# Optimization experiments

Hardware: AMD Instinct MI355X
Metric: run time of the kernel (lower is better)

The kernel has to match this reference:

```python
import jax, jax.numpy as jnp
import numpy as np

N, C, H = 256, 128, 4
D = C // H


def setup_inputs() -> dict:
    key = jax.random.key(0)
    ks = jax.random.split(key, 7)
    pair_rep = jax.random.normal(ks[0], (N, N, C), dtype=jnp.float32)
    distance_matrix = jax.random.normal(ks[1], (N, N), dtype=jnp.float32)
    Wqkv = jax.random.normal(ks[2], (C, 3 * C), dtype=jnp.float32) * (1.0 / np.sqrt(C))
    bqkv = jax.random.normal(ks[3], (3 * C,), dtype=jnp.float32) * 0.02
    Wout = jax.random.normal(ks[4], (C, C), dtype=jnp.float32) * (1.0 / np.sqrt(C))
    bout = jax.random.normal(ks[5], (C,), dtype=jnp.float32) * 0.02
    dscale = jnp.ones((1,), dtype=jnp.float32)
    mask = jax.random.randint(ks[6], (N, N), 0, 2).astype(jnp.bool_)
    return {"pair_rep": pair_rep, "distance_matrix": distance_matrix, "Wqkv": Wqkv,
            "bqkv": bqkv, "Wout": Wout, "bout": bout, "dscale": dscale, "mask": mask}


def reference(pair_rep, distance_matrix, Wqkv, bqkv, Wout, bout, dscale, mask):
    n = pair_rep.shape[0]
    qkv = pair_rep @ Wqkv + bqkv                      # [n,n,3c]
    q, k, v = jnp.split(qkv, 3, axis=-1)
    q = q.reshape(n, n, H, D)
    k = k.reshape(n, n, H, D)
    v = v.reshape(n, n, H, D)
    # scores[h,i,j,k] = q[i,j,h,:] . k[i,k,h,:] / sqrt(D)
    scores = jnp.einsum('ijhd,ikhd->hijk', q, k) / np.sqrt(D)
    bias = (dscale[0] * distance_matrix)[None, None, :, :]   # [1,1,n,n]
    scores = scores + bias
    scores = jnp.where(mask[None, None, :, :], -jnp.inf, scores)
    attn = jax.nn.softmax(scores, axis=-1)            # [H,n,n,n]
    out = jnp.einsum('hijk,ikhd->ijhd', attn, v).reshape(n, n, C)
    return out @ Wout + bout
```

## Files before the change

kernel.cpp:

```cpp
#include <hip/hip_runtime.h>
#include <hip/hip_bf16.h>
#include <math.h>

#define NN 256
#define CC 128
#define HH 4
#define DD 32

typedef uint4 u128;
typedef __bf16 bf16x8 __attribute__((ext_vector_type(8)));
typedef float f32x4 __attribute__((ext_vector_type(4)));

#define LOG2E 1.4426950408889634f
#define QSC (0.17677669529663687f * LOG2E)

__global__ __launch_bounds__(256) void prep_kernel(
    const float* __restrict__ dm, const int* __restrict__ mask,
    const float* __restrict__ dscale,
    const float* __restrict__ Wqkv, const float* __restrict__ Wout,
    float* __restrict__ bias2,
    __hip_bfloat16* __restrict__ Wt_qkv, __hip_bfloat16* __restrict__ Wt_out)
{
    const int b = blockIdx.x, t = threadIdx.x;
    if (b < 256) {
        const int j = b, k = t;
        int idx = j * 256 + k;
        float v = mask[idx] ? -INFINITY : dscale[0] * dm[idx] * LOG2E;
        int c = k >> 5, bb = (k >> 4) & 1, quad = (k >> 2) & 3, r = k & 3;
        int dst = ((((c * 2 + bb) * 16 + (j >> 4)) * 64) + quad * 16 + (j & 15)) * 4 + r;
        bias2[dst] = v;
    } else if (b < 448) {
        int idx = (b - 256) * 256 + t;
        int n = idx >> 7, k = idx & 127;
        Wt_qkv[idx] = __float2bfloat16(Wqkv[(size_t)k * 384 + n]);
    } else {
        int idx = (b - 448) * 256 + t;
        int n = idx >> 7, k = idx & 127;
        Wt_out[idx] = __float2bfloat16(Wout[(size_t)k * CC + n]);
    }
}

__global__ __launch_bounds__(512, 4) void qkv_mfma_kernel(
    const float* __restrict__ A,
    const __hip_bfloat16* __restrict__ Bt,
    const float* __restrict__ bias,
    __hip_bfloat16* __restrict__ out)
{
    __shared__ __align__(16) __hip_bfloat16 As[128][136];
    __shared__ __align__(16) __hip_bfloat16 Bs[96][136];
    const int t = threadIdx.x;
    const int m0 = blockIdx.x * 128;
    const int n0 = blockIdx.y * 96;

    #pragma unroll
    for (int it = 0; it < 8; ++it) {
        int idx = it * 512 + t;
        int r = idx >> 5, c4 = (idx & 31) * 4;
        float4 v = *(const float4*)(A + (size_t)(m0 + r) * CC + c4);
        __hip_bfloat162 a01 = __float22bfloat162_rn(float2{v.x, v.y});
        __hip_bfloat162 a23 = __float22bfloat162_rn(float2{v.z, v.w});
        uint2 pk;
        pk.x = *(unsigned int*)&a01;
        pk.y = *(unsigned int*)&a23;
        *(uint2*)&As[r][c4] = pk;
    }
    #pragma unroll
    for (int it = 0; it < 3; ++it) {
        int idx = it * 512 + t;
        int n = idx >> 4, c8 = (idx & 15) * 8;
        *(u128*)&Bs[n][c8] = *(const u128*)(Bt + (size_t)(n0 + n) * CC + c8);
    }
    __syncthreads();

    const int w = t >> 6, lane = t & 63;
    const int n16 = lane & 15, quad = lane >> 4;
    const int mw = (w & 3) * 32, nw = (w >> 2) * 48;

    bf16x8 pf[2][4];
    #pragma unroll
    for (int mt = 0; mt < 2; ++mt)
        #pragma unroll
        for (int ks = 0; ks < 4; ++ks)
            pf[mt][ks] = *(const bf16x8*)&As[mw + mt * 16 + n16][ks * 32 + quad * 8];

    f32x4 acc[2][3];
    #pragma unroll
    for (int mt = 0; mt < 2; ++mt)
        #pragma unroll
        for (int nt = 0; nt < 3; ++nt) acc[mt][nt] = (f32x4){0.f, 0.f, 0.f, 0.f};

    #pragma unroll
    for (int nt = 0; nt < 3; ++nt) {
        bf16x8 wf[4];
        #pragma unroll
        for (int ks = 0; ks < 4; ++ks)
            wf[ks] = *(const bf16x8*)&Bs[nw + nt * 16 + n16][ks * 32 + quad * 8];
        #pragma unroll
        for (int ks = 0; ks < 4; ++ks)
            #pragma unroll
            for (int mt = 0; mt < 2; ++mt)
                acc[mt][nt] = __builtin_amdgcn_mfma_f32_16x16x32_bf16(wf[ks], pf[mt][ks], acc[mt][nt], 0, 0, 0);
    }

    #pragma unroll
    for (int nt = 0; nt < 3; ++nt) {
        int nbase = n0 + nw + nt * 16 + quad * 4;
        float4 b4 = *(const float4*)(bias + nbase);
        float sc = (nbase < CC) ? QSC : 1.0f;
        #pragma unroll
        for (int mt = 0; mt < 2; ++mt) {
            int m = m0 + mw + mt * 16 + n16;
            __hip_bfloat162 h01 = __float22bfloat162_rn(float2{(acc[mt][nt][0] + b4.x) * sc, (acc[mt][nt][1] + b4.y) * sc});
            __hip_bfloat162 h23 = __float22bfloat162_rn(float2{(acc[mt][nt][2] + b4.z) * sc, (acc[mt][nt][3] + b4.w) * sc});
            uint2 pk;
            pk.x = *(unsigned int*)&h01;
            pk.y = *(unsigned int*)&h23;
            *(uint2*)&out[(size_t)m * 384 + nbase] = pk;
        }
    }
}

__global__ __launch_bounds__(512, 8) void attn_mfma_kernel(
    const __hip_bfloat16* __restrict__ qkv,
    const float* __restrict__ bias2,
    __hip_bfloat16* __restrict__ attn_out)
{
    __shared__ __align__(16) __hip_bfloat16 Ks[NN][40];
    __shared__ __align__(16) __hip_bfloat16 VTs[DD][264];

    const int bi = blockIdx.x;
    const int i = bi >> 2, h = bi & 3;
    const int t = threadIdx.x;

    {
        const int r = t >> 1, half = t & 1;
        const __hip_bfloat16* base = qkv + (size_t)(i * NN + r) * 384 + h * DD;
        const u128* ksrc = (const u128*)(base + CC) + half * 2;
        u128* kdst = (u128*)&Ks[r][0] + half * 2;
        kdst[0] = ksrc[0];
        kdst[1] = ksrc[1];
        const u128* vsrc = (const u128*)(base + 2 * CC) + half * 2;
        u128 vr[2];
        vr[0] = vsrc[0];
        vr[1] = vsrc[1];
        const __hip_bfloat16* vh = (const __hip_bfloat16*)vr;
        const int pr = (r & ~0x1F) | ((r & 0xC) << 1) | ((r & 0x10) >> 2) | (r & 0x3);
        #pragma unroll
        for (int dd = 0; dd < 16; ++dd) VTs[half * 16 + dd][pr] = vh[dd];
    }
    __syncthreads();

    const int w = t >> 6, lane = t & 63;
    const int n16 = lane & 15, quad = lane >> 4;

    #pragma unroll
    for (int jt = 0; jt < 2; ++jt) {
        const int j0 = w * 32 + jt * 16;
        const int j = j0 + n16;
        const int jblk = w * 2 + jt;

        bf16x8 qa = *(const bf16x8*)(qkv + (size_t)(i * NN + j) * 384 + h * DD + quad * 8);
        const float4* bb = (const float4*)bias2;

        f32x4 sm = {0.f, 0.f, 0.f, 0.f};
        f32x4 o0 = {0.f, 0.f, 0.f, 0.f}, o1 = {0.f, 0.f, 0.f, 0.f};

        #pragma unroll 2
        for (int c = 0; c < 8; ++c) {
            float4 b0 = bb[((c * 2 + 0) * 16 + jblk) * 64 + lane];
            float4 b1 = bb[((c * 2 + 1) * 16 + jblk) * 64 + lane];
            bf16x8 kb0 = *(const bf16x8*)&Ks[c * 32 + n16][quad * 8];
            bf16x8 kb1 = *(const bf16x8*)&Ks[c * 32 + 16 + n16][quad * 8];
            f32x4 s0 = __builtin_amdgcn_mfma_f32_16x16x32_bf16(
                kb0, qa, (f32x4){b0.x, b0.y, b0.z, b0.w}, 0, 0, 0);
            f32x4 s1 = __builtin_amdgcn_mfma_f32_16x16x32_bf16(
                kb1, qa, (f32x4){b1.x, b1.y, b1.z, b1.w}, 0, 0, 0);

            float p0 = __builtin_amdgcn_exp2f(s0[0]);
            float p1 = __builtin_amdgcn_exp2f(s0[1]);
            float p2 = __builtin_amdgcn_exp2f(s0[2]);
            float p3 = __builtin_amdgcn_exp2f(s0[3]);
            float p4 = __builtin_amdgcn_exp2f(s1[0]);
            float p5 = __builtin_amdgcn_exp2f(s1[1]);
            float p6 = __builtin_amdgcn_exp2f(s1[2]);
            float p7 = __builtin_amdgcn_exp2f(s1[3]);
            sm[0] += p0 + p4;
            sm[1] += p1 + p5;
            sm[2] += p2 + p6;
            sm[3] += p3 + p7;

            __hip_bfloat162 q01 = __float22bfloat162_rn(float2{p0, p1});
            __hip_bfloat162 q23 = __float22bfloat162_rn(float2{p2, p3});
            __hip_bfloat162 q45 = __float22bfloat162_rn(float2{p4, p5});
            __hip_bfloat162 q67 = __float22bfloat162_rn(float2{p6, p7});
            u128 pk;
            pk.x = *(unsigned int*)&q01;
            pk.y = *(unsigned int*)&q23;
            pk.z = *(unsigned int*)&q45;
            pk.w = *(unsigned int*)&q67;
            bf16x8 pa = *(bf16x8*)&pk;

            bf16x8 vb0 = *(const bf16x8*)&VTs[n16][c * 32 + quad * 8];
            bf16x8 vb1 = *(const bf16x8*)&VTs[16 + n16][c * 32 + quad * 8];
            o0 = __builtin_amdgcn_mfma_f32_16x16x32_bf16(vb0, pa, o0, 0, 0, 0);
            o1 = __builtin_amdgcn_mfma_f32_16x16x32_bf16(vb1, pa, o1, 0, 0, 0);
        }

        float sum = (sm[0] + sm[1]) + (sm[2] + sm[3]);
        sum += __shfl_xor(sum, 16);
        sum += __shfl_xor(sum, 32);
        float inv = 1.0f / sum;

        __hip_bfloat16* obase = attn_out + (size_t)(i * NN + j) * CC + h * DD + quad * 4;
        {
            __hip_bfloat162 h01 = __float22bfloat162_rn(float2{o0[0] * inv, o0[1] * inv});
            __hip_bfloat162 h23 = __float22bfloat162_rn(float2{o0[2] * inv, o0[3] * inv});
            uint2 pk;
            pk.x = *(unsigned int*)&h01;
            pk.y = *(unsigned int*)&h23;
            *(uint2*)(obase) = pk;
        }
        {
            __hip_bfloat162 h01 = __float22bfloat162_rn(float2{o1[0] * inv, o1[1] * inv});
            __hip_bfloat162 h23 = __float22bfloat162_rn(float2{o1[2] * inv, o1[3] * inv});
            uint2 pk;
            pk.x = *(unsigned int*)&h01;
            pk.y = *(unsigned int*)&h23;
            *(uint2*)(obase + 16) = pk;
        }
    }
}

__global__ __launch_bounds__(512, 4) void out_mfma_kernel(
    const __hip_bfloat16* __restrict__ A,
    const __hip_bfloat16* __restrict__ Bt,
    const float* __restrict__ bias,
    float* __restrict__ out)
{
    __shared__ __align__(16) __hip_bfloat16 As[128][136];
    __shared__ __align__(16) __hip_bfloat16 Bs[128][136];
    const int t = threadIdx.x;
    const int m0 = blockIdx.x * 128;

    #pragma unroll
    for (int it = 0; it < 4; ++it) {
        int idx = it * 512 + t;
        int r = idx >> 4, c8 = (idx & 15) * 8;
        *(u128*)&As[r][c8] = *(const u128*)(A + (size_t)(m0 + r) * CC + c8);
    }
    #pragma unroll
    for (int it = 0; it < 4; ++it) {
        int idx = it * 512 + t;
        int n = idx >> 4, c8 = (idx & 15) * 8;
        *(u128*)&Bs[n][c8] = *(const u128*)(Bt + (size_t)n * CC + c8);
    }
    __syncthreads();

    const int w = t >> 6, lane = t & 63;
    const int n16 = lane & 15, quad = lane >> 4;
    const int mw = (w & 3) * 32, nw = (w >> 2) * 64;

    bf16x8 pf[2][4];
    #pragma unroll
    for (int mt = 0; mt < 2; ++mt)
        #pragma unroll
        for (int ks = 0; ks < 4; ++ks)
            pf[mt][ks] = *(const bf16x8*)&As[mw + mt * 16 + n16][ks * 32 + quad * 8];

    f32x4 acc[2][4];
    #pragma unroll
    for (int mt = 0; mt < 2; ++mt)
        #pragma unroll
        for (int nt = 0; nt < 4; ++nt) acc[mt][nt] = (f32x4){0.f, 0.f, 0.f, 0.f};

    #pragma unroll
    for (int nt = 0; nt < 4; ++nt) {
        bf16x8 wf[4];
        #pragma unroll
        for (int ks = 0; ks < 4; ++ks)
            wf[ks] = *(const bf16x8*)&Bs[nw + nt * 16 + n16][ks * 32 + quad * 8];
        #pragma unroll
        for (int ks = 0; ks < 4; ++ks)
            #pragma unroll
            for (int mt = 0; mt < 2; ++mt)
                acc[mt][nt] = __builtin_amdgcn_mfma_f32_16x16x32_bf16(wf[ks], pf[mt][ks], acc[mt][nt], 0, 0, 0);
    }

    #pragma unroll
    for (int nt = 0; nt < 4; ++nt) {
        int nbase = nw + nt * 16 + quad * 4;
        float4 b4 = *(const float4*)(bias + nbase);
        #pragma unroll
        for (int mt = 0; mt < 2; ++mt) {
            int m = m0 + mw + mt * 16 + n16;
            float4 ov;
            ov.x = acc[mt][nt][0] + b4.x;
            ov.y = acc[mt][nt][1] + b4.y;
            ov.z = acc[mt][nt][2] + b4.z;
            ov.w = acc[mt][nt][3] + b4.w;
            *(float4*)&out[(size_t)m * CC + nbase] = ov;
        }
    }
}

extern "C" void kernel_launch(void* const* d_in, const int* in_sizes, int n_in,
                              void* d_out, int out_size, void* d_ws, size_t ws_size,
                              hipStream_t stream) {
    const float* pair_rep = (const float*)d_in[0];
    const float* dm       = (const float*)d_in[1];
    const float* Wqkv     = (const float*)d_in[2];
    const float* bqkv     = (const float*)d_in[3];
    const float* Wout     = (const float*)d_in[4];
    const float* bout     = (const float*)d_in[5];
    const float* dscale   = (const float*)d_in[6];
    const int*   mask     = (const int*)d_in[7];
    float* out = (float*)d_out;

    char* p = (char*)d_ws;
    float* bias2 = (float*)p;                 p += (size_t)NN * NN * 4;
    __hip_bfloat16* Wt_qkv = (__hip_bfloat16*)p;  p += (size_t)384 * CC * 2;
    __hip_bfloat16* Wt_out = (__hip_bfloat16*)p;  p += (size_t)CC * CC * 2;
    __hip_bfloat16* qkv  = (__hip_bfloat16*)p;    p += (size_t)65536 * 384 * 2;
    __hip_bfloat16* attn = (__hip_bfloat16*)p;

    prep_kernel<<<dim3(512), dim3(256), 0, stream>>>(dm, mask, dscale, Wqkv, Wout, bias2, Wt_qkv, Wt_out);
    qkv_mfma_kernel<<<dim3(512, 4), dim3(512), 0, stream>>>(pair_rep, Wt_qkv, bqkv, qkv);
    attn_mfma_kernel<<<dim3(1024), dim3(512), 0, stream>>>(qkv, bias2, attn);
    out_mfma_kernel<<<dim3(512), dim3(512), 0, stream>>>(attn, Wt_out, bout, out);
}
```

Baseline: 160.8 us.

## Load A tile once per QKV block and loop over output column chunks

The QKV projection grid drops from 512x4 to 512 blocks. Each block converts its fp32 input rows to bf16 in shared memory once, then loops over the four 96-column weight chunks, prefetching the next chunk into registers while writing the current outputs. This removes the fourfold re-read of the fp32 pair representation. Global loads in the QKV and output GEMMs are also batched into registers before the shared-memory stores to increase memory-level parallelism. The cost is fewer blocks, more serial work per block, and a lower occupancy hint.

```diff
diff --git a/kernel.cpp b/kernel.cpp
--- a/kernel.cpp
+++ b/kernel.cpp
@@ -40,7 +40,7 @@
     }
 }
 
-__global__ __launch_bounds__(512, 4) void qkv_mfma_kernel(
+__global__ __launch_bounds__(512, 2) void qkv_mfma_kernel(
     const float* __restrict__ A,
     const __hip_bfloat16* __restrict__ Bt,
     const float* __restrict__ bias,
@@ -50,15 +50,20 @@
     __shared__ __align__(16) __hip_bfloat16 Bs[96][136];
     const int t = threadIdx.x;
     const int m0 = blockIdx.x * 128;
-    const int n0 = blockIdx.y * 96;
-
+
+    float4 va[8];
     #pragma unroll
     for (int it = 0; it < 8; ++it) {
         int idx = it * 512 + t;
         int r = idx >> 5, c4 = (idx & 31) * 4;
-        float4 v = *(const float4*)(A + (size_t)(m0 + r) * CC + c4);
-        __hip_bfloat162 a01 = __float22bfloat162_rn(float2{v.x, v.y});
-        __hip_bfloat162 a23 = __float22bfloat162_rn(float2{v.z, v.w});
+        va[it] = *(const float4*)(A + (size_t)(m0 + r) * CC + c4);
+    }
+    #pragma unroll
+    for (int it = 0; it < 8; ++it) {
+        int idx = it * 512 + t;
+        int r = idx >> 5, c4 = (idx & 31) * 4;
+        __hip_bfloat162 a01 = __float22bfloat162_rn(float2{va[it].x, va[it].y});
+        __hip_bfloat162 a23 = __float22bfloat162_rn(float2{va[it].z, va[it].w});
         uint2 pk;
         pk.x = *(unsigned int*)&a01;
         pk.y = *(unsigned int*)&a23;
@@ -68,7 +73,7 @@
     for (int it = 0; it < 3; ++it) {
         int idx = it * 512 + t;
         int n = idx >> 4, c8 = (idx & 15) * 8;
-        *(u128*)&Bs[n][c8] = *(const u128*)(Bt + (size_t)(n0 + n) * CC + c8);
+        *(u128*)&Bs[n][c8] = *(const u128*)(Bt + (size_t)n * CC + c8);
     }
     __syncthreads();
 
@@ -83,39 +88,64 @@
         for (int ks = 0; ks < 4; ++ks)
             pf[mt][ks] = *(const bf16x8*)&As[mw + mt * 16 + n16][ks * 32 + quad * 8];
 
-    f32x4 acc[2][3];
-    #pragma unroll
-    for (int mt = 0; mt < 2; ++mt)
-        #pragma unroll
-        for (int nt = 0; nt < 3; ++nt) acc[mt][nt] = (f32x4){0.f, 0.f, 0.f, 0.f};
-
-    #pragma unroll
-    for (int nt = 0; nt < 3; ++nt) {
-        bf16x8 wf[4];
-        #pragma unroll
-        for (int ks = 0; ks < 4; ++ks)
-            wf[ks] = *(const bf16x8*)&Bs[nw + nt * 16 + n16][ks * 32 + quad * 8];
-        #pragma unroll
-        for (int ks = 0; ks < 4; ++ks)
-            #pragma unroll
-            for (int mt = 0; mt < 2; ++mt)
-                acc[mt][nt] = __builtin_amdgcn_mfma_f32_16x16x32_bf16(wf[ks], pf[mt][ks], acc[mt][nt], 0, 0, 0);
-    }
-
-    #pragma unroll
-    for (int nt = 0; nt < 3; ++nt) {
-        int nbase = n0 + nw + nt * 16 + quad * 4;
-        float4 b4 = *(const float4*)(bias + nbase);
-        float sc = (nbase < CC) ? QSC : 1.0f;
-        #pragma unroll
-        for (int mt = 0; mt < 2; ++mt) {
-            int m = m0 + mw + mt * 16 + n16;
-            __hip_bfloat162 h01 = __float22bfloat162_rn(float2{(acc[mt][nt][0] + b4.x) * sc, (acc[mt][nt][1] + b4.y) * sc});
-            __hip_bfloat162 h23 = __float22bfloat162_rn(float2{(acc[mt][nt][2] + b4.z) * sc, (acc[mt][nt][3] + b4.w) * sc});
-            uint2 pk;
-            pk.x = *(unsigned int*)&h01;
-            pk.y = *(unsigned int*)&h23;
-            *(uint2*)&out[(size_t)m * 384 + nbase] = pk;
+    for (int nc = 0; nc < 4; ++nc) {
+        const int n0 = nc * 96;
+
+        f32x4 acc[2][3];
+        #pragma unroll
+        for (int mt = 0; mt < 2; ++mt)
+            #pragma unroll
+            for (int nt = 0; nt < 3; ++nt) acc[mt][nt] = (f32x4){0.f, 0.f, 0.f, 0.f};
+
+        #pragma unroll
+        for (int nt = 0; nt < 3; ++nt) {
+            bf16x8 wf[4];
+            #pragma unroll
+            for (int ks = 0; ks < 4; ++ks)
+                wf[ks] = *(const bf16x8*)&Bs[nw + nt * 16 + n16][ks * 32 + quad * 8];
+            #pragma unroll
+            for (int ks = 0; ks < 4; ++ks)
+                #pragma unroll
+                for (int mt = 0; mt < 2; ++mt)
+                    acc[mt][nt] = __builtin_amdgcn_mfma_f32_16x16x32_bf16(wf[ks], pf[mt][ks], acc[mt][nt], 0, 0, 0);
+        }
+        __syncthreads();
+
+        u128 breg[3];
+        if (nc < 3) {
+            #pragma unroll
+            for (int it = 0; it < 3; ++it) {
+                int idx = it * 512 + t;
+                int n = idx >> 4, c8 = (idx & 15) * 8;
+                breg[it] = *(const u128*)(Bt + (size_t)(n0 + 96 + n) * CC + c8);
+            }
+        }
+
+        #pragma unroll
+        for (int nt = 0; nt < 3; ++nt) {
+            int nbase = n0 + nw + nt * 16 + quad * 4;
+            float4 b4 = *(const float4*)(bias + nbase);
+            float sc = (nbase < CC) ? QSC : 1.0f;
+            #pragma unroll
+            for (int mt = 0; mt < 2; ++mt) {
+                int m = m0 + mw + mt * 16 + n16;
+                __hip_bfloat162 h01 = __float22bfloat162_rn(float2{(acc[mt][nt][0] + b4.x) * sc, (acc[mt][nt][1] + b4.y) * sc});
+                __hip_bfloat162 h23 = __float22bfloat162_rn(float2{(acc[mt][nt][2] + b4.z) * sc, (acc[mt][nt][3] + b4.w) * sc});
+                uint2 pk;
+                pk.x = *(unsigned int*)&h01;
+                pk.y = *(unsigned int*)&h23;
+                *(uint2*)&out[(size_t)m * 384 + nbase] = pk;
+            }
+        }
+
+        if (nc < 3) {
+            #pragma unroll
+            for (int it = 0; it < 3; ++it) {
+                int idx = it * 512 + t;
+                int n = idx >> 4, c8 = (idx & 15) * 8;
+                *(u128*)&Bs[n][c8] = breg[it];
+            }
+            __syncthreads();
         }
     }
 }
@@ -242,17 +272,30 @@
     const int t = threadIdx.x;
     const int m0 = blockIdx.x * 128;
 
+    u128 ra[4], rb[4];
     #pragma unroll
     for (int it = 0; it < 4; ++it) {
         int idx = it * 512 + t;
         int r = idx >> 4, c8 = (idx & 15) * 8;
-        *(u128*)&As[r][c8] = *(const u128*)(A + (size_t)(m0 + r) * CC + c8);
+        ra[it] = *(const u128*)(A + (size_t)(m0 + r) * CC + c8);
     }
     #pragma unroll
     for (int it = 0; it < 4; ++it) {
         int idx = it * 512 + t;
         int n = idx >> 4, c8 = (idx & 15) * 8;
-        *(u128*)&Bs[n][c8] = *(const u128*)(Bt + (size_t)n * CC + c8);
+        rb[it] = *(const u128*)(Bt + (size_t)n * CC + c8);
+    }
+    #pragma unroll
+    for (int it = 0; it < 4; ++it) {
+        int idx = it * 512 + t;
+        int r = idx >> 4, c8 = (idx & 15) * 8;
+        *(u128*)&As[r][c8] = ra[it];
+    }
+    #pragma unroll
+    for (int it = 0; it < 4; ++it) {
+        int idx = it * 512 + t;
+        int n = idx >> 4, c8 = (idx & 15) * 8;
+        *(u128*)&Bs[n][c8] = rb[it];
     }
     __syncthreads();
 
@@ -324,7 +367,7 @@
     __hip_bfloat16* attn = (__hip_bfloat16*)p;
 
     prep_kernel<<<dim3(512), dim3(256), 0, stream>>>(dm, mask, dscale, Wqkv, Wout, bias2, Wt_qkv, Wt_out);
-    qkv_mfma_kernel<<<dim3(512, 4), dim3(512), 0, stream>>>(pair_rep, Wt_qkv, bqkv, qkv);
+    qkv_mfma_kernel<<<dim3(512), dim3(512), 0, stream>>>(pair_rep, Wt_qkv, bqkv, qkv);
     attn_mfma_kernel<<<dim3(1024), dim3(512), 0, stream>>>(qkv, bias2, attn);
     out_mfma_kernel<<<dim3(512), dim3(512), 0, stream>>>(attn, Wt_out, bout, out);
 }
```

Result: faster. 146.4 us (-8.9%).

## Fuse QKV projection into attention kernel, drop qkv intermediate buffer

Applied to the files above, without the earlier changes.

Removes the separate QKV GEMM kernel. Each attention block (one row i, one head h) now projects its own Q, K and V slices straight from pair_rep into shared memory with MFMA, so the 50MB bf16 qkv intermediate is never written to or read back from global memory. In exchange, each pair_rep row is read once per head (four times in total), and the block index order is changed so that blocks sharing a row i are spaced 256 apart. The out-projection kernel also gathers all global loads into registers before writing shared memory, so the loads can be in flight together.

```diff
diff --git a/kernel.cpp b/kernel.cpp
--- a/kernel.cpp
+++ b/kernel.cpp
@@ -40,118 +40,95 @@
     }
 }
 
-__global__ __launch_bounds__(512, 4) void qkv_mfma_kernel(
-    const float* __restrict__ A,
-    const __hip_bfloat16* __restrict__ Bt,
-    const float* __restrict__ bias,
-    __hip_bfloat16* __restrict__ out)
-{
-    __shared__ __align__(16) __hip_bfloat16 As[128][136];
-    __shared__ __align__(16) __hip_bfloat16 Bs[96][136];
-    const int t = threadIdx.x;
-    const int m0 = blockIdx.x * 128;
-    const int n0 = blockIdx.y * 96;
-
-    #pragma unroll
-    for (int it = 0; it < 8; ++it) {
-        int idx = it * 512 + t;
-        int r = idx >> 5, c4 = (idx & 31) * 4;
-        float4 v = *(const float4*)(A + (size_t)(m0 + r) * CC + c4);
-        __hip_bfloat162 a01 = __float22bfloat162_rn(float2{v.x, v.y});
-        __hip_bfloat162 a23 = __float22bfloat162_rn(float2{v.z, v.w});
-        uint2 pk;
-        pk.x = *(unsigned int*)&a01;
-        pk.y = *(unsigned int*)&a23;
-        *(uint2*)&As[r][c4] = pk;
-    }
-    #pragma unroll
-    for (int it = 0; it < 3; ++it) {
-        int idx = it * 512 + t;
-        int n = idx >> 4, c8 = (idx & 15) * 8;
-        *(u128*)&Bs[n][c8] = *(const u128*)(Bt + (size_t)(n0 + n) * CC + c8);
-    }
-    __syncthreads();
-
-    const int w = t >> 6, lane = t & 63;
-    const int n16 = lane & 15, quad = lane >> 4;
-    const int mw = (w & 3) * 32, nw = (w >> 2) * 48;
-
-    bf16x8 pf[2][4];
-    #pragma unroll
-    for (int mt = 0; mt < 2; ++mt)
-        #pragma unroll
-        for (int ks = 0; ks < 4; ++ks)
-            pf[mt][ks] = *(const bf16x8*)&As[mw + mt * 16 + n16][ks * 32 + quad * 8];
-
-    f32x4 acc[2][3];
-    #pragma unroll
-    for (int mt = 0; mt < 2; ++mt)
-        #pragma unroll
-        for (int nt = 0; nt < 3; ++nt) acc[mt][nt] = (f32x4){0.f, 0.f, 0.f, 0.f};
-
-    #pragma unroll
-    for (int nt = 0; nt < 3; ++nt) {
-        bf16x8 wf[4];
-        #pragma unroll
-        for (int ks = 0; ks < 4; ++ks)
-            wf[ks] = *(const bf16x8*)&Bs[nw + nt * 16 + n16][ks * 32 + quad * 8];
-        #pragma unroll
-        for (int ks = 0; ks < 4; ++ks)
-            #pragma unroll
-            for (int mt = 0; mt < 2; ++mt)
-                acc[mt][nt] = __builtin_amdgcn_mfma_f32_16x16x32_bf16(wf[ks], pf[mt][ks], acc[mt][nt], 0, 0, 0);
-    }
-
-    #pragma unroll
-    for (int nt = 0; nt < 3; ++nt) {
-        int nbase = n0 + nw + nt * 16 + quad * 4;
-        float4 b4 = *(const float4*)(bias + nbase);
-        float sc = (nbase < CC) ? QSC : 1.0f;
-        #pragma unroll
-        for (int mt = 0; mt < 2; ++mt) {
-            int m = m0 + mw + mt * 16 + n16;
-            __hip_bfloat162 h01 = __float22bfloat162_rn(float2{(acc[mt][nt][0] + b4.x) * sc, (acc[mt][nt][1] + b4.y) * sc});
-            __hip_bfloat162 h23 = __float22bfloat162_rn(float2{(acc[mt][nt][2] + b4.z) * sc, (acc[mt][nt][3] + b4.w) * sc});
-            uint2 pk;
-            pk.x = *(unsigned int*)&h01;
-            pk.y = *(unsigned int*)&h23;
-            *(uint2*)&out[(size_t)m * 384 + nbase] = pk;
-        }
-    }
-}
-
-__global__ __launch_bounds__(512, 8) void attn_mfma_kernel(
-    const __hip_bfloat16* __restrict__ qkv,
+__global__ __launch_bounds__(512, 4) void attn_fused_kernel(
+    const float* __restrict__ pair,
+    const __hip_bfloat16* __restrict__ Wt,
+    const float* __restrict__ bqkv,
     const float* __restrict__ bias2,
     __hip_bfloat16* __restrict__ attn_out)
 {
     __shared__ __align__(16) __hip_bfloat16 Ks[NN][40];
     __shared__ __align__(16) __hip_bfloat16 VTs[DD][264];
+    __shared__ __align__(16) __hip_bfloat16 Qs[NN][40];
 
     const int bi = blockIdx.x;
-    const int i = bi >> 2, h = bi & 3;
+    const int i = bi & 255, h = bi >> 8;
     const int t = threadIdx.x;
-
-    {
-        const int r = t >> 1, half = t & 1;
-        const __hip_bfloat16* base = qkv + (size_t)(i * NN + r) * 384 + h * DD;
-        const u128* ksrc = (const u128*)(base + CC) + half * 2;
-        u128* kdst = (u128*)&Ks[r][0] + half * 2;
-        kdst[0] = ksrc[0];
-        kdst[1] = ksrc[1];
-        const u128* vsrc = (const u128*)(base + 2 * CC) + half * 2;
-        u128 vr[2];
-        vr[0] = vsrc[0];
-        vr[1] = vsrc[1];
-        const __hip_bfloat16* vh = (const __hip_bfloat16*)vr;
-        const int pr = (r & ~0x1F) | ((r & 0xC) << 1) | ((r & 0x10) >> 2) | (r & 0x3);
-        #pragma unroll
-        for (int dd = 0; dd < 16; ++dd) VTs[half * 16 + dd][pr] = vh[dd];
-    }
-    __syncthreads();
-
     const int w = t >> 6, lane = t & 63;
     const int n16 = lane & 15, quad = lane >> 4;
+
+    bf16x8 pf[2][4];
+    #pragma unroll
+    for (int jt2 = 0; jt2 < 2; ++jt2) {
+        const float* prow = pair + ((size_t)i * NN + w * 32 + jt2 * 16 + n16) * CC;
+        float4 x[4], y[4];
+        #pragma unroll
+        for (int ks = 0; ks < 4; ++ks) {
+            x[ks] = *(const float4*)(prow + ks * 32 + quad * 8);
+            y[ks] = *(const float4*)(prow + ks * 32 + quad * 8 + 4);
+        }
+        #pragma unroll
+        for (int ks = 0; ks < 4; ++ks) {
+            __hip_bfloat162 a01 = __float22bfloat162_rn(float2{x[ks].x, x[ks].y});
+            __hip_bfloat162 a23 = __float22bfloat162_rn(float2{x[ks].z, x[ks].w});
+            __hip_bfloat162 a45 = __float22bfloat162_rn(float2{y[ks].x, y[ks].y});
+            __hip_bfloat162 a67 = __float22bfloat162_rn(float2{y[ks].z, y[ks].w});
+            u128 pk;
+            pk.x = *(unsigned int*)&a01;
+            pk.y = *(unsigned int*)&a23;
+            pk.z = *(unsigned int*)&a45;
+            pk.w = *(unsigned int*)&a67;
+            pf[jt2][ks] = *(bf16x8*)&pk;
+        }
+    }
+
+    #pragma unroll
+    for (int tt = 0; tt < 3; ++tt) {
+        const int tb = (tt == 0) ? 128 : (tt == 1) ? 256 : 0;
+        bf16x8 wf[2][4];
+        #pragma unroll
+        for (int db = 0; db < 2; ++db)
+            #pragma unroll
+            for (int ks = 0; ks < 4; ++ks)
+                wf[db][ks] = *(const bf16x8*)(Wt + (size_t)(tb + h * 32 + db * 16 + n16) * CC + ks * 32 + quad * 8);
+        float b0 = bqkv[tb + h * 32 + n16];
+        float b1 = bqkv[tb + h * 32 + 16 + n16];
+
+        f32x4 acc[2][2];
+        #pragma unroll
+        for (int jt2 = 0; jt2 < 2; ++jt2)
+            #pragma unroll
+            for (int db = 0; db < 2; ++db) acc[jt2][db] = (f32x4){0.f, 0.f, 0.f, 0.f};
+        #pragma unroll
+        for (int ks = 0; ks < 4; ++ks)
+            #pragma unroll
+            for (int jt2 = 0; jt2 < 2; ++jt2)
+                #pragma unroll
+                for (int db = 0; db < 2; ++db)
+                    acc[jt2][db] = __builtin_amdgcn_mfma_f32_16x16x32_bf16(pf[jt2][ks], wf[db][ks], acc[jt2][db], 0, 0, 0);
+
+        #pragma unroll
+        for (int jt2 = 0; jt2 < 2; ++jt2)
+            #pragma unroll
+            for (int db = 0; db < 2; ++db) {
+                float bb = db ? b1 : b0;
+                #pragma unroll
+                for (int r = 0; r < 4; ++r) {
+                    float v = acc[jt2][db][r] + bb;
+                    int j = w * 32 + jt2 * 16 + quad * 4 + r;
+                    int d = db * 16 + n16;
+                    if (tt == 0) {
+                        Ks[j][d] = __float2bfloat16(v);
+                    } else if (tt == 1) {
+                        int pj = w * 32 + quad * 8 + jt2 * 4 + r;
+                        VTs[d][pj] = __float2bfloat16(v);
+                    } else {
+                        Qs[j][d] = __float2bfloat16(v * QSC);
+                    }
+                }
+            }
+    }
+    __syncthreads();
 
     #pragma unroll
     for (int jt = 0; jt < 2; ++jt) {
@@ -159,7 +136,7 @@
         const int j = j0 + n16;
         const int jblk = w * 2 + jt;
 
-        bf16x8 qa = *(const bf16x8*)(qkv + (size_t)(i * NN + j) * 384 + h * DD + quad * 8);
+        bf16x8 qa = *(const bf16x8*)&Qs[j][quad * 8];
         const float4* bb = (const float4*)bias2;
 
         f32x4 sm = {0.f, 0.f, 0.f, 0.f};
@@ -242,17 +219,30 @@
     const int t = threadIdx.x;
     const int m0 = blockIdx.x * 128;
 
+    u128 ra[4], rb[4];
     #pragma unroll
     for (int it = 0; it < 4; ++it) {
         int idx = it * 512 + t;
         int r = idx >> 4, c8 = (idx & 15) * 8;
-        *(u128*)&As[r][c8] = *(const u128*)(A + (size_t)(m0 + r) * CC + c8);
+        ra[it] = *(const u128*)(A + (size_t)(m0 + r) * CC + c8);
     }
     #pragma unroll
     for (int it = 0; it < 4; ++it) {
         int idx = it * 512 + t;
         int n = idx >> 4, c8 = (idx & 15) * 8;
-        *(u128*)&Bs[n][c8] = *(const u128*)(Bt + (size_t)n * CC + c8);
+        rb[it] = *(const u128*)(Bt + (size_t)n * CC + c8);
+    }
+    #pragma unroll
+    for (int it = 0; it < 4; ++it) {
+        int idx = it * 512 + t;
+        int r = idx >> 4, c8 = (idx & 15) * 8;
+        *(u128*)&As[r][c8] = ra[it];
+    }
+    #pragma unroll
+    for (int it = 0; it < 4; ++it) {
+        int idx = it * 512 + t;
+        int n = idx >> 4, c8 = (idx & 15) * 8;
+        *(u128*)&Bs[n][c8] = rb[it];
     }
     __syncthreads();
 
@@ -320,11 +310,9 @@
     float* bias2 = (float*)p;                 p += (size_t)NN * NN * 4;
     __hip_bfloat16* Wt_qkv = (__hip_bfloat16*)p;  p += (size_t)384 * CC * 2;
     __hip_bfloat16* Wt_out = (__hip_bfloat16*)p;  p += (size_t)CC * CC * 2;
-    __hip_bfloat16* qkv  = (__hip_bfloat16*)p;    p += (size_t)65536 * 384 * 2;
     __hip_bfloat16* attn = (__hip_bfloat16*)p;
 
     prep_kernel<<<dim3(512), dim3(256), 0, stream>>>(dm, mask, dscale, Wqkv, Wout, bias2, Wt_qkv, Wt_out);
-    qkv_mfma_kernel<<<dim3(512, 4), dim3(512), 0, stream>>>(pair_rep, Wt_qkv, bqkv, qkv);
-    attn_mfma_kernel<<<dim3(1024), dim3(512), 0, stream>>>(qkv, bias2, attn);
+    attn_fused_kernel<<<dim3(1024), dim3(512), 0, stream>>>(pair_rep, Wt_qkv, bqkv, bias2, attn);
     out_mfma_kernel<<<dim3(512), dim3(512), 0, stream>>>(attn, Wt_out, bout, out);
 }
```

New measurement: 148.7 us. 1.08x faster.
